# Kernel optimization log

Measured on AMD Instinct MI355X. Metric: run time of the kernel, lower is better.

The kernel has to match this reference:

```python
import jax, jax.numpy as jnp
import numpy as np

BETA = 0.25
EPS = 1e-10


def setup_inputs() -> dict:
    key = jax.random.key(0)
    k1, k2 = jax.random.split(key)
    B, D, K = 32768, 512, 8192
    a = jax.random.normal(k1, (B, D), dtype=jnp.float32)
    # torch init: uniform(-1/K, 1/K)
    codebook = jax.random.uniform(k2, (K, D), dtype=jnp.float32,
                                  minval=-1.0 / K, maxval=1.0 / K)
    return {"a": a, "codebook": codebook}


def reference(a, codebook):
    # a: [B, D], codebook: [K, D]
    B = a.shape[0]
    K = codebook.shape[0]
    # squared-distance via a2 + e2 - 2*a.E^T (no [B,K,D] intermediate)
    a2 = jnp.sum(a * a, axis=1, keepdims=True)            # [B, 1]
    e2 = jnp.sum(codebook * codebook, axis=1)[None, :]    # [1, K]
    dist = a2 + e2 - 2.0 * (a @ codebook.T)               # [B, K]
    idx = jnp.argmin(dist, axis=1)                        # [B] int
    z_q = codebook[idx]                                   # [B, D]
    # straight-through estimator
    z = a + jax.lax.stop_gradient(z_q - a)
    commit_loss = BETA * jnp.mean((a - jax.lax.stop_gradient(z_q)) ** 2)
    codebook_loss = jnp.mean((jax.lax.stop_gradient(a) - z_q) ** 2)
    # usage stats (no_grad in torch)
    usage = jnp.zeros((K,), a.dtype).at[idx].add(1.0) / B  # mean of one-hot
    perplexity = jnp.exp(-jnp.sum(usage * jnp.log(usage + EPS)))
    used_codes = jnp.sum(usage > 0).astype(a.dtype)
    usage_mean = jnp.mean(usage)
    return (idx, z, commit_loss, codebook_loss, perplexity, used_codes, usage_mean)
```

## Files before the change

kernel.cpp:

```cpp
#include <hip/hip_runtime.h>
#include <stdint.h>

#define D_DIM 512
#define ESTRIDE 528
#define SPLIT_K 384
#define DELTA 8.0e-4f
#define MAXC 48

typedef unsigned long long u64;
typedef float f32x4 __attribute__((ext_vector_type(4)));
typedef short s16x8 __attribute__((ext_vector_type(8)));

static __device__ inline unsigned short f2bf(float x) {
  unsigned u = __float_as_uint(x);
  u = (u + 0x7FFFu + ((u >> 16) & 1u)) >> 16;
  return (unsigned short)u;
}
static __device__ inline unsigned mono(float f) {
  unsigned u = __float_as_uint(f);
  return (u & 0x80000000u) ? ~u : (u | 0x80000000u);
}
static __device__ inline float unmono(unsigned m) {
  return __uint_as_float((m & 0x80000000u) ? (m & 0x7FFFFFFFu) : ~m);
}

__global__ void k_init(int* __restrict__ counts, int K) {
  int i = blockIdx.x * blockDim.x + threadIdx.x;
  if (i < K) counts[i] = 0;
}

__global__ void k_rowsq(const float* __restrict__ X, float* __restrict__ out, int nrows) {
  int t = threadIdx.x;
  int row = blockIdx.x * 4 + (t >> 6);
  int l = t & 63;
  if (row >= nrows) return;
  int b = l >> 4;
  int L = l & 15;
  const float* p = X + (size_t)row * D_DIM + b * 128 + L;
  float v[8];
#pragma unroll
  for (int j = 0; j < 8; ++j) {
    float x = p[16 * j];
    float sq = x * x;
    asm volatile("" : "+v"(sq));
    v[j] = sq;
  }
  float s = ((v[0] + v[1]) + (v[2] + v[3])) + ((v[4] + v[5]) + (v[6] + v[7]));
  s += __shfl_xor(s, 8, 64);
  s += __shfl_xor(s, 4, 64);
  s += __shfl_xor(s, 2, 64);
  s += __shfl_xor(s, 1, 64);
  s += __shfl_xor(s, 16, 64);
  s += __shfl_xor(s, 32, 64);
  if (l == 0) out[row] = s;
}

__global__ void k_ebf(const float* __restrict__ E, unsigned short* __restrict__ Ebf, int n8) {
  int i = blockIdx.x * blockDim.x + threadIdx.x;
  if (i >= n8) return;
  const float4 f0 = ((const float4*)E)[i * 2];
  const float4 f1 = ((const float4*)E)[i * 2 + 1];
  s16x8 o;
  o[0] = (short)f2bf(f0.x); o[1] = (short)f2bf(f0.y);
  o[2] = (short)f2bf(f0.z); o[3] = (short)f2bf(f0.w);
  o[4] = (short)f2bf(f1.x); o[5] = (short)f2bf(f1.y);
  o[6] = (short)f2bf(f1.z); o[7] = (short)f2bf(f1.w);
  ((s16x8*)Ebf)[i] = o;
}

__global__ void k_eskew(const float* __restrict__ E, float* __restrict__ Es, int n4) {
  int i = blockIdx.x * blockDim.x + threadIdx.x;
  if (i >= n4) return;
  int row = i >> 7;
  int c = i & 127;
  float4 v = ((const float4*)(E + (size_t)row * D_DIM))[c];
  ((float4*)(Es + (size_t)row * ESTRIDE))[c] = v;
}

__global__ __launch_bounds__(512) void k_screen(
    const float* __restrict__ A, const unsigned short* __restrict__ Ebf,
    const float* __restrict__ e2, int* __restrict__ cand_cnt,
    unsigned short* __restrict__ cand, int K) {
  __shared__ unsigned runmin[128];
  __shared__ unsigned cnt[128];
  __shared__ unsigned short list[128 * MAXC];
  __shared__ __align__(16) char Alds[128 * 1024];

  const int t = threadIdx.x;
  const int m0 = blockIdx.x * 128;

  if (t < 128) { runmin[t] = 0xFFFFFFFFu; cnt[t] = 0; }

  {
    int row = t >> 2;
    int s4 = t & 3;
    const float* ar = A + (size_t)(m0 + row) * D_DIM;
#pragma unroll
    for (int c = 0; c < 16; ++c) {
      int ch = s4 * 16 + c;
      float4 f0 = *(const float4*)(ar + ch * 8);
      float4 f1 = *(const float4*)(ar + ch * 8 + 4);
      s16x8 o;
      o[0] = (short)f2bf(f0.x); o[1] = (short)f2bf(f0.y);
      o[2] = (short)f2bf(f0.z); o[3] = (short)f2bf(f0.w);
      o[4] = (short)f2bf(f1.x); o[5] = (short)f2bf(f1.y);
      o[6] = (short)f2bf(f1.z); o[7] = (short)f2bf(f1.w);
      int off = ((row * 64 + ch) * 16) ^ ((row & 7) << 4);
      *(s16x8*)(Alds + off) = o;
    }
  }
  __syncthreads();

  const int lane = t & 63;
  const int wid = t >> 6;
  const int wm = wid >> 2;
  const int wn = wid & 3;
  const int l15 = lane & 15;
  const int lhi = lane >> 4;

  for (int n0 = 0; n0 < K; n0 += 128) {
    f32x4 acc[4][2];
#pragma unroll
    for (int r = 0; r < 4; ++r)
#pragma unroll
      for (int c = 0; c < 2; ++c) acc[r][c] = (f32x4){0.f, 0.f, 0.f, 0.f};
    const unsigned short* B0 = Ebf + (size_t)(n0 + wn * 32 + l15) * D_DIM + lhi * 8;
    const unsigned short* B1 = B0 + 16 * D_DIM;
#pragma unroll
    for (int dk = 0; dk < 16; ++dk) {
      s16x8 b0 = *(const s16x8*)(B0 + dk * 32);
      s16x8 b1 = *(const s16x8*)(B1 + dk * 32);
      s16x8 af[4];
#pragma unroll
      for (int r = 0; r < 4; ++r) {
        int row = wm * 64 + r * 16 + l15;
        int off = ((row * 64 + dk * 4 + lhi) * 16) ^ ((row & 7) << 4);
        af[r] = *(const s16x8*)(Alds + off);
      }
#pragma unroll
      for (int r = 0; r < 4; ++r) {
        acc[r][0] = __builtin_amdgcn_mfma_f32_16x16x32_bf16(af[r], b0, acc[r][0], 0, 0, 0);
        acc[r][1] = __builtin_amdgcn_mfma_f32_16x16x32_bf16(af[r], b1, acc[r][1], 0, 0, 0);
      }
    }
    float e2c0 = e2[n0 + wn * 32 + l15];
    float e2c1 = e2[n0 + wn * 32 + 16 + l15];
#pragma unroll
    for (int r = 0; r < 4; ++r)
#pragma unroll
      for (int g = 0; g < 4; ++g) {
        float s0 = fmaf(-2.f, acc[r][0][g], e2c0);
        float s1 = fmaf(-2.f, acc[r][1][g], e2c1);
        int row = wm * 64 + r * 16 + lhi * 4 + g;
        float mn = fminf(s0, s1);
        mn = fminf(mn, __shfl_xor(mn, 1, 64));
        mn = fminf(mn, __shfl_xor(mn, 2, 64));
        mn = fminf(mn, __shfl_xor(mn, 4, 64));
        mn = fminf(mn, __shfl_xor(mn, 8, 64));
        if (l15 == 0) atomicMin(&runmin[row], mono(mn));
        float thr = unmono(runmin[row]) + DELTA;
        if (s0 <= thr) {
          unsigned p = atomicAdd(&cnt[row], 1u);
          if (p < MAXC) list[row * MAXC + p] = (unsigned short)(n0 + wn * 32 + l15);
        }
        if (s1 <= thr) {
          unsigned p = atomicAdd(&cnt[row], 1u);
          if (p < MAXC) list[row * MAXC + p] = (unsigned short)(n0 + wn * 32 + 16 + l15);
        }
      }
  }
  __syncthreads();
  {
    int row = t >> 2;
    unsigned c = cnt[row];
    if ((t & 3) == 0) cand_cnt[m0 + row] = (int)c;
    unsigned cc = c < MAXC ? c : MAXC;
    for (unsigned p = t & 3; p < cc; p += 4)
      cand[(size_t)(m0 + row) * MAXC + p] = list[row * MAXC + p];
  }
}

static __device__ inline u64 exact_pack(const float* __restrict__ ar,
                                        const float* __restrict__ er,
                                        float a2r, float e2k, int k) {
  float acc1 = 0.f, acc2 = 0.f;
  for (int d = 0; d < SPLIT_K; d += 4) {
    float4 a = *(const float4*)(ar + d);
    float4 e = *(const float4*)(er + d);
    acc1 = fmaf(a.x, e.x, acc1); acc1 = fmaf(a.y, e.y, acc1);
    acc1 = fmaf(a.z, e.z, acc1); acc1 = fmaf(a.w, e.w, acc1);
  }
  for (int d = SPLIT_K; d < D_DIM; d += 4) {
    float4 a = *(const float4*)(ar + d);
    float4 e = *(const float4*)(er + d);
    acc2 = fmaf(a.x, e.x, acc2); acc2 = fmaf(a.y, e.y, acc2);
    acc2 = fmaf(a.z, e.z, acc2); acc2 = fmaf(a.w, e.w, acc2);
  }
  float M = acc1 + acc2;
  float S = a2r + e2k;
  float s = fmaf(-2.f, M, S);
  return ((u64)mono(s) << 32) | (unsigned)k;
}

__global__ __launch_bounds__(256) void k_rescore(
    const float* __restrict__ A, const float* __restrict__ Eskew,
    const float* __restrict__ a2, const float* __restrict__ e2,
    const int* __restrict__ cand_cnt, const unsigned short* __restrict__ cand,
    float* __restrict__ out_idx, float* __restrict__ out_z,
    float* __restrict__ rowsum, int* __restrict__ counts, int K) {
  int lane = threadIdx.x & 63;
  int r = blockIdx.x * 4 + (threadIdx.x >> 6);
  int c = cand_cnt[r];
  const float* ar = A + (size_t)r * D_DIM;
  float a2r = a2[r];
  u64 best = ~0ULL;
  if (c <= MAXC) {
    if (lane < c) {
      int k = cand[(size_t)r * MAXC + lane];
      best = exact_pack(ar, Eskew + (size_t)k * ESTRIDE, a2r, e2[k], k);
    }
  } else {
    for (int k = lane; k < K; k += 64) {
      u64 p = exact_pack(ar, Eskew + (size_t)k * ESTRIDE, a2r, e2[k], k);
      if (p < best) best = p;
    }
  }
#pragma unroll
  for (int m = 1; m < 64; m <<= 1) {
    u64 o = __shfl_xor(best, m, 64);
    if (o < best) best = o;
  }
  int idx = (int)(unsigned)(best & 0xFFFFFFFFULL);

  const float4* pa = (const float4*)(ar) + lane * 2;
  const float4* pe = (const float4*)(Eskew + (size_t)idx * ESTRIDE) + lane * 2;
  float4* pz = (float4*)(out_z + (size_t)r * D_DIM) + lane * 2;
  float ls = 0.f;
#pragma unroll
  for (int q = 0; q < 2; ++q) {
    float4 a = pa[q];
    float4 e = pe[q];
    float4 z;
    z.x = a.x + (e.x - a.x);
    z.y = a.y + (e.y - a.y);
    z.z = a.z + (e.z - a.z);
    z.w = a.w + (e.w - a.w);
    pz[q] = z;
    float dx = a.x - e.x, dy = a.y - e.y, dz = a.z - e.z, dw = a.w - e.w;
    ls += dx * dx + dy * dy + dz * dz + dw * dw;
  }
#pragma unroll
  for (int m = 1; m < 64; m <<= 1) ls += __shfl_xor(ls, m, 64);
  if (lane == 0) {
    out_idx[r] = (float)idx;
    rowsum[r] = ls;
    atomicAdd(&counts[idx], 1);
  }
}

#define KTILE(D0, ACC)                                                          \
  {                                                                             \
    int r = t >> 2;                                                             \
    int c4 = (t & 3) << 2;                                                      \
    float4 va = *(const float4*)(A + (size_t)(m0 + r) * D_DIM + (D0) + c4);     \
    As[c4 + 0][r] = va.x; As[c4 + 1][r] = va.y;                                 \
    As[c4 + 2][r] = va.z; As[c4 + 3][r] = va.w;                                 \
    float4 vb = *(const float4*)(E + (size_t)(n0 + r) * D_DIM + (D0) + c4);     \
    Es[c4 + 0][r] = vb.x; Es[c4 + 1][r] = vb.y;                                 \
    Es[c4 + 2][r] = vb.z; Es[c4 + 3][r] = vb.w;                                 \
    __syncthreads();                                                            \
    _Pragma("unroll")                                                           \
    for (int dd = 0; dd < 16; ++dd) {                                           \
      float af[4], bf[8];                                                       \
      *(float4*)af = *(const float4*)(&As[dd][ty * 4]);                         \
      *(float4*)bf = *(const float4*)(&Es[dd][tx * 4]);                         \
      *(float4*)(bf + 4) = *(const float4*)(&Es[dd][64 + tx * 4]);              \
      _Pragma("unroll")                                                         \
      for (int i = 0; i < 4; ++i)                                               \
        _Pragma("unroll")                                                       \
        for (int j = 0; j < 8; ++j)                                             \
          ACC[i][j] = fmaf(af[i], bf[j], ACC[i][j]);                            \
    }                                                                           \
    __syncthreads();                                                            \
  }

__global__ __launch_bounds__(512) void k_argmin_f32(
    const float* __restrict__ A, const float* __restrict__ E,
    const float* __restrict__ a2, const float* __restrict__ e2,
    float* __restrict__ out_idx, int* __restrict__ idx_ws, int K) {
  __shared__ float As[16][128];
  __shared__ float Es[16][128];
  const int m0 = blockIdx.x * 128;
  const int t = threadIdx.x;
  const int tx = t & 15;
  const int ty = t >> 4;
  float a2l[4];
#pragma unroll
  for (int i = 0; i < 4; ++i) a2l[i] = a2[m0 + ty * 4 + i];
  u64 best[4];
#pragma unroll
  for (int i = 0; i < 4; ++i) best[i] = ~0ULL;
  for (int n0 = 0; n0 < K; n0 += 128) {
    float acc1[4][8], acc2[4][8];
#pragma unroll
    for (int i = 0; i < 4; ++i)
#pragma unroll
      for (int j = 0; j < 8; ++j) { acc1[i][j] = 0.f; acc2[i][j] = 0.f; }
    for (int d0 = 0; d0 < SPLIT_K; d0 += 16) KTILE(d0, acc1)
    for (int d0 = SPLIT_K; d0 < D_DIM; d0 += 16) KTILE(d0, acc2)
    float e2l[8];
#pragma unroll
    for (int j = 0; j < 8; ++j) {
      int cl = (j < 4) ? (tx * 4 + j) : (64 + tx * 4 + (j - 4));
      e2l[j] = e2[n0 + cl];
    }
#pragma unroll
    for (int i = 0; i < 4; ++i) {
#pragma unroll
      for (int j = 0; j < 8; ++j) {
        int cl = (j < 4) ? (tx * 4 + j) : (64 + tx * 4 + (j - 4));
        float S = a2l[i] + e2l[j];
        float m = acc1[i][j] + acc2[i][j];
        float s = fmaf(-2.f, m, S);
        u64 p = ((u64)mono(s) << 32) | (unsigned)(n0 + cl);
        if (p < best[i]) best[i] = p;
      }
    }
  }
#pragma unroll
  for (int m = 1; m < 16; m <<= 1) {
#pragma unroll
    for (int i = 0; i < 4; ++i) {
      u64 o = __shfl_xor(best[i], m, 64);
      if (o < best[i]) best[i] = o;
    }
  }
  if (tx == 0) {
#pragma unroll
    for (int i = 0; i < 4; ++i) {
      int row = m0 + ty * 4 + i;
      int idx = (int)(unsigned)(best[i] & 0xFFFFFFFFULL);
      out_idx[row] = (float)idx;
      idx_ws[row] = idx;
    }
  }
}

__global__ void k_gather(const float* __restrict__ A, const float* __restrict__ E,
                         const int* __restrict__ idx_ws,
                         float* __restrict__ out_z, float* __restrict__ rowsum,
                         int* __restrict__ counts) {
  int b = blockIdx.x;
  int t = threadIdx.x;
  int idx = idx_ws[b];
  const float4* pa = (const float4*)(A + (size_t)b * D_DIM);
  const float4* pe = (const float4*)(E + (size_t)idx * D_DIM);
  float4 a = pa[t];
  float4 e = pe[t];
  float4 z;
  z.x = a.x + (e.x - a.x);
  z.y = a.y + (e.y - a.y);
  z.z = a.z + (e.z - a.z);
  z.w = a.w + (e.w - a.w);
  ((float4*)(out_z + (size_t)b * D_DIM))[t] = z;
  float dx = a.x - e.x, dy = a.y - e.y, dz = a.z - e.z, dw = a.w - e.w;
  float ls = dx * dx + dy * dy + dz * dz + dw * dw;
#pragma unroll
  for (int off = 32; off > 0; off >>= 1) ls += __shfl_down(ls, off, 64);
  __shared__ float wsum[2];
  if ((t & 63) == 0) wsum[t >> 6] = ls;
  __syncthreads();
  if (t == 0) {
    rowsum[b] = wsum[0] + wsum[1];
    atomicAdd(&counts[idx], 1);
  }
}

__global__ void k_stats(const int* __restrict__ counts, const float* __restrict__ rowsum,
                        float* __restrict__ out_sc, int B, int K) {
  int t = threadIdx.x;
  double ent = 0.0, tot = 0.0, S = 0.0;
  int used = 0;
  for (int k = t; k < K; k += 256) {
    int c = counts[k];
    double u = (double)c / (double)B;
    ent += u * log(u + 1e-10);
    tot += u;
    used += (c > 0) ? 1 : 0;
  }
  for (int b = t; b < B; b += 256) S += (double)rowsum[b];
  __shared__ double se[256];
  __shared__ double st[256];
  __shared__ double ss[256];
  __shared__ int su[256];
  se[t] = ent; st[t] = tot; ss[t] = S; su[t] = used;
  __syncthreads();
  for (int s = 128; s > 0; s >>= 1) {
    if (t < s) { se[t] += se[t + s]; st[t] += st[t + s]; ss[t] += ss[t + s]; su[t] += su[t + s]; }
    __syncthreads();
  }
  if (t == 0) {
    double Sm = ss[0];
    double N = (double)B * (double)D_DIM;
    out_sc[0] = (float)(0.25 * Sm / N);
    out_sc[1] = (float)(Sm / N);
    out_sc[2] = (float)exp(-se[0]);
    out_sc[3] = (float)su[0];
    out_sc[4] = (float)(st[0] / (double)K);
  }
}

extern "C" void kernel_launch(void* const* d_in, const int* in_sizes, int n_in,
                              void* d_out, int out_size, void* d_ws, size_t ws_size,
                              hipStream_t stream) {
  const float* A = (const float*)d_in[0];
  const float* E = (const float*)d_in[1];
  const int B = in_sizes[0] / D_DIM;
  const int K = in_sizes[1] / D_DIM;

  float* out = (float*)d_out;
  float* out_idx = out;
  float* out_z = out + B;
  float* out_sc = out + B + (size_t)B * D_DIM;

  char* ws = (char*)d_ws;
  size_t off = 0;
  float* a2 = (float*)(ws + off); off += (size_t)B * 4;
  float* e2 = (float*)(ws + off); off += (size_t)K * 4;
  int* counts = (int*)(ws + off); off += (size_t)K * 4;
  float* rowsum = (float*)(ws + off); off += (size_t)B * 4;
  int* idx_ws = (int*)(ws + off); off += (size_t)B * 4;
  int* cand_cnt = (int*)(ws + off); off += (size_t)B * 4;
  unsigned short* cand = (unsigned short*)(ws + off); off += (size_t)B * MAXC * 2;
  unsigned short* Ebf = (unsigned short*)(ws + off); off += (size_t)K * D_DIM * 2;
  float* Eskew = (float*)(ws + off); off += (size_t)K * ESTRIDE * 4;
  const size_t need = off;

  k_init<<<(K + 255) / 256, 256, 0, stream>>>(counts, K);
  k_rowsq<<<(B + 3) / 4, 256, 0, stream>>>(A, a2, B);
  k_rowsq<<<(K + 3) / 4, 256, 0, stream>>>(E, e2, K);

  if (ws_size >= need) {
    int n8 = K * D_DIM / 8;
    k_ebf<<<(n8 + 255) / 256, 256, 0, stream>>>(E, Ebf, n8);
    int n4 = K * D_DIM / 4;
    k_eskew<<<(n4 + 255) / 256, 256, 0, stream>>>(E, Eskew, n4);
    k_screen<<<B / 128, 512, 0, stream>>>(A, Ebf, e2, cand_cnt, cand, K);
    k_rescore<<<B / 4, 256, 0, stream>>>(A, Eskew, a2, e2, cand_cnt, cand,
                                         out_idx, out_z, rowsum, counts, K);
  } else {
    k_argmin_f32<<<B / 128, 512, 0, stream>>>(A, E, a2, e2, out_idx, idx_ws, K);
    k_gather<<<B, 128, 0, stream>>>(A, E, idx_ws, out_z, rowsum, counts);
  }
  k_stats<<<1, 256, 0, stream>>>(counts, rowsum, out_sc, B, K);
}
```

Before: 1.039 ms.

## Pad bf16 codebook rows, prefetch B fragments, widen LDS swizzle, cap occupancy

The bf16 codebook copy now uses a padded row stride of 544 elements, likely to avoid cache-channel or bank aliasing on strided row loads. In the screening kernel, all 16 k-steps of B fragments are loaded into registers before the MFMA loop, so global loads are issued together rather than interleaved with compute. The A tile LDS XOR swizzle is widened from 8 to 16 rows to cut bank conflicts. Launch bounds now request 2 blocks per CU, which raises register pressure alongside the 32 extra vector registers of prefetched fragments.

```diff
diff --git a/kernel.cpp b/kernel.cpp
--- a/kernel.cpp
+++ b/kernel.cpp
@@ -2,6 +2,7 @@
 #include <stdint.h>
 
 #define D_DIM 512
+#define EBFS 544
 #define ESTRIDE 528
 #define SPLIT_K 384
 #define DELTA 8.0e-4f
@@ -58,14 +59,16 @@
 __global__ void k_ebf(const float* __restrict__ E, unsigned short* __restrict__ Ebf, int n8) {
   int i = blockIdx.x * blockDim.x + threadIdx.x;
   if (i >= n8) return;
-  const float4 f0 = ((const float4*)E)[i * 2];
-  const float4 f1 = ((const float4*)E)[i * 2 + 1];
+  int row = i >> 6;
+  int ch = i & 63;
+  const float4 f0 = *(const float4*)(E + (size_t)row * D_DIM + ch * 8);
+  const float4 f1 = *(const float4*)(E + (size_t)row * D_DIM + ch * 8 + 4);
   s16x8 o;
   o[0] = (short)f2bf(f0.x); o[1] = (short)f2bf(f0.y);
   o[2] = (short)f2bf(f0.z); o[3] = (short)f2bf(f0.w);
   o[4] = (short)f2bf(f1.x); o[5] = (short)f2bf(f1.y);
   o[6] = (short)f2bf(f1.z); o[7] = (short)f2bf(f1.w);
-  ((s16x8*)Ebf)[i] = o;
+  *(s16x8*)(Ebf + (size_t)row * EBFS + ch * 8) = o;
 }
 
 __global__ void k_eskew(const float* __restrict__ E, float* __restrict__ Es, int n4) {
@@ -77,7 +80,7 @@
   ((float4*)(Es + (size_t)row * ESTRIDE))[c] = v;
 }
 
-__global__ __launch_bounds__(512) void k_screen(
+__global__ __launch_bounds__(512, 2) void k_screen(
     const float* __restrict__ A, const unsigned short* __restrict__ Ebf,
     const float* __restrict__ e2, int* __restrict__ cand_cnt,
     unsigned short* __restrict__ cand, int K) {
@@ -105,7 +108,7 @@
       o[2] = (short)f2bf(f0.z); o[3] = (short)f2bf(f0.w);
       o[4] = (short)f2bf(f1.x); o[5] = (short)f2bf(f1.y);
       o[6] = (short)f2bf(f1.z); o[7] = (short)f2bf(f1.w);
-      int off = ((row * 64 + ch) * 16) ^ ((row & 7) << 4);
+      int off = ((row * 64 + ch) * 16) ^ ((row & 15) << 4);
       *(s16x8*)(Alds + off) = o;
     }
   }
@@ -119,28 +122,34 @@
   const int lhi = lane >> 4;
 
   for (int n0 = 0; n0 < K; n0 += 128) {
+    s16x8 bb0[16], bb1[16];
+    {
+      const unsigned short* B0 = Ebf + (size_t)(n0 + wn * 32 + l15) * EBFS + lhi * 8;
+      const unsigned short* B1 = B0 + 16 * EBFS;
+#pragma unroll
+      for (int dk = 0; dk < 16; ++dk) {
+        bb0[dk] = *(const s16x8*)(B0 + dk * 32);
+        bb1[dk] = *(const s16x8*)(B1 + dk * 32);
+      }
+    }
     f32x4 acc[4][2];
 #pragma unroll
     for (int r = 0; r < 4; ++r)
 #pragma unroll
       for (int c = 0; c < 2; ++c) acc[r][c] = (f32x4){0.f, 0.f, 0.f, 0.f};
-    const unsigned short* B0 = Ebf + (size_t)(n0 + wn * 32 + l15) * D_DIM + lhi * 8;
-    const unsigned short* B1 = B0 + 16 * D_DIM;
 #pragma unroll
     for (int dk = 0; dk < 16; ++dk) {
-      s16x8 b0 = *(const s16x8*)(B0 + dk * 32);
-      s16x8 b1 = *(const s16x8*)(B1 + dk * 32);
       s16x8 af[4];
 #pragma unroll
       for (int r = 0; r < 4; ++r) {
         int row = wm * 64 + r * 16 + l15;
-        int off = ((row * 64 + dk * 4 + lhi) * 16) ^ ((row & 7) << 4);
+        int off = ((row * 64 + dk * 4 + lhi) * 16) ^ ((row & 15) << 4);
         af[r] = *(const s16x8*)(Alds + off);
       }
 #pragma unroll
       for (int r = 0; r < 4; ++r) {
-        acc[r][0] = __builtin_amdgcn_mfma_f32_16x16x32_bf16(af[r], b0, acc[r][0], 0, 0, 0);
-        acc[r][1] = __builtin_amdgcn_mfma_f32_16x16x32_bf16(af[r], b1, acc[r][1], 0, 0, 0);
+        acc[r][0] = __builtin_amdgcn_mfma_f32_16x16x32_bf16(af[r], bb0[dk], acc[r][0], 0, 0, 0);
+        acc[r][1] = __builtin_amdgcn_mfma_f32_16x16x32_bf16(af[r], bb1[dk], acc[r][1], 0, 0, 0);
       }
     }
     float e2c0 = e2[n0 + wn * 32 + l15];
@@ -432,7 +441,7 @@
   int* idx_ws = (int*)(ws + off); off += (size_t)B * 4;
   int* cand_cnt = (int*)(ws + off); off += (size_t)B * 4;
   unsigned short* cand = (unsigned short*)(ws + off); off += (size_t)B * MAXC * 2;
-  unsigned short* Ebf = (unsigned short*)(ws + off); off += (size_t)K * D_DIM * 2;
+  unsigned short* Ebf = (unsigned short*)(ws + off); off += (size_t)K * EBFS * 2;
   float* Eskew = (float*)(ws + off); off += (size_t)K * ESTRIDE * 4;
   const size_t need = off;
 
```

Result: faster. 910.2 us (-12.4%).

## Stage codebook tiles into LDS via async global_load_lds with double buffering

Applied to the files above, without the earlier changes.

The screening GEMM now streams pre-tiled bf16 codebook chunks into a double-buffered LDS region using global_load_lds, instead of each wave reading B fragments straight from global memory. A new prep kernel writes the codebook in a chunk-major tiled layout and, in the same pass, produces the fp32 skewed copy and zeroes the counts, replacing three small launches. The A swizzle is widened to reduce LDS bank conflicts. The tile loop is hardcoded to K=8192, and a block-wide barrier now runs every k-step, which adds sync overhead.

```diff
diff --git a/kernel.cpp b/kernel.cpp
--- a/kernel.cpp
+++ b/kernel.cpp
@@ -27,6 +27,29 @@
 __global__ void k_init(int* __restrict__ counts, int K) {
   int i = blockIdx.x * blockDim.x + threadIdx.x;
   if (i < K) counts[i] = 0;
+}
+
+__global__ void k_prep(const float* __restrict__ E, unsigned short* __restrict__ Ebf2,
+                       float* __restrict__ Eskew, int* __restrict__ counts, int K) {
+  int i = blockIdx.x * blockDim.x + threadIdx.x;
+  if (i < K) counts[i] = 0;
+  if (i >= K * 64) return;
+  int row = i >> 6;
+  int ch = i & 63;
+  const float* src = E + (size_t)row * D_DIM + ch * 8;
+  float4 f0 = *(const float4*)(src);
+  float4 f1 = *(const float4*)(src + 4);
+  s16x8 o;
+  o[0] = (short)f2bf(f0.x); o[1] = (short)f2bf(f0.y);
+  o[2] = (short)f2bf(f0.z); o[3] = (short)f2bf(f0.w);
+  o[4] = (short)f2bf(f1.x); o[5] = (short)f2bf(f1.y);
+  o[6] = (short)f2bf(f1.z); o[7] = (short)f2bf(f1.w);
+  size_t slot = ((size_t)(row >> 7) * 16 + (size_t)(ch >> 2)) * 512 +
+                (size_t)(row & 127) * 4 + (size_t)(ch & 3);
+  *(s16x8*)(Ebf2 + slot * 8) = o;
+  float* dst = Eskew + (size_t)row * ESTRIDE + ch * 8;
+  *(float4*)(dst) = f0;
+  *(float4*)(dst + 4) = f1;
 }
 
 __global__ void k_rowsq(const float* __restrict__ X, float* __restrict__ out, int nrows) {
@@ -55,36 +78,15 @@
   if (l == 0) out[row] = s;
 }
 
-__global__ void k_ebf(const float* __restrict__ E, unsigned short* __restrict__ Ebf, int n8) {
-  int i = blockIdx.x * blockDim.x + threadIdx.x;
-  if (i >= n8) return;
-  const float4 f0 = ((const float4*)E)[i * 2];
-  const float4 f1 = ((const float4*)E)[i * 2 + 1];
-  s16x8 o;
-  o[0] = (short)f2bf(f0.x); o[1] = (short)f2bf(f0.y);
-  o[2] = (short)f2bf(f0.z); o[3] = (short)f2bf(f0.w);
-  o[4] = (short)f2bf(f1.x); o[5] = (short)f2bf(f1.y);
-  o[6] = (short)f2bf(f1.z); o[7] = (short)f2bf(f1.w);
-  ((s16x8*)Ebf)[i] = o;
-}
-
-__global__ void k_eskew(const float* __restrict__ E, float* __restrict__ Es, int n4) {
-  int i = blockIdx.x * blockDim.x + threadIdx.x;
-  if (i >= n4) return;
-  int row = i >> 7;
-  int c = i & 127;
-  float4 v = ((const float4*)(E + (size_t)row * D_DIM))[c];
-  ((float4*)(Es + (size_t)row * ESTRIDE))[c] = v;
-}
-
 __global__ __launch_bounds__(512) void k_screen(
-    const float* __restrict__ A, const unsigned short* __restrict__ Ebf,
+    const float* __restrict__ A, const unsigned short* __restrict__ Ebf2,
     const float* __restrict__ e2, int* __restrict__ cand_cnt,
     unsigned short* __restrict__ cand, int K) {
   __shared__ unsigned runmin[128];
   __shared__ unsigned cnt[128];
   __shared__ unsigned short list[128 * MAXC];
   __shared__ __align__(16) char Alds[128 * 1024];
+  __shared__ __align__(16) char Blds[2 * 8192];
 
   const int t = threadIdx.x;
   const int m0 = blockIdx.x * 128;
@@ -105,11 +107,10 @@
       o[2] = (short)f2bf(f0.z); o[3] = (short)f2bf(f0.w);
       o[4] = (short)f2bf(f1.x); o[5] = (short)f2bf(f1.y);
       o[6] = (short)f2bf(f1.z); o[7] = (short)f2bf(f1.w);
-      int off = ((row * 64 + ch) * 16) ^ ((row & 7) << 4);
+      int off = ((row * 64 + ch) * 16) ^ ((row & 15) << 4);
       *(s16x8*)(Alds + off) = o;
     }
   }
-  __syncthreads();
 
   const int lane = t & 63;
   const int wid = t >> 6;
@@ -118,23 +119,40 @@
   const int l15 = lane & 15;
   const int lhi = lane >> 4;
 
-  for (int n0 = 0; n0 < K; n0 += 128) {
+#define ISSUE_CHUNK(C)                                                          \
+  {                                                                             \
+    const unsigned short* _src = Ebf2 + ((size_t)(C) * 512 + t) * 8;            \
+    __builtin_amdgcn_global_load_lds(                                           \
+        (const __attribute__((address_space(1))) unsigned int*)_src,            \
+        (__attribute__((address_space(3))) unsigned int*)(Blds + ((C) & 1) * 8192 + wid * 1024), \
+        16, 0, 0);                                                              \
+  }
+
+  ISSUE_CHUNK(0)
+  __syncthreads();
+
+  for (int tile = 0; tile < 64; ++tile) {
+    const int n0 = tile * 128;
+
     f32x4 acc[4][2];
 #pragma unroll
     for (int r = 0; r < 4; ++r)
 #pragma unroll
       for (int c = 0; c < 2; ++c) acc[r][c] = (f32x4){0.f, 0.f, 0.f, 0.f};
-    const unsigned short* B0 = Ebf + (size_t)(n0 + wn * 32 + l15) * D_DIM + lhi * 8;
-    const unsigned short* B1 = B0 + 16 * D_DIM;
-#pragma unroll
-    for (int dk = 0; dk < 16; ++dk) {
-      s16x8 b0 = *(const s16x8*)(B0 + dk * 32);
-      s16x8 b1 = *(const s16x8*)(B1 + dk * 32);
+
+#pragma unroll
+    for (int kk = 0; kk < 16; ++kk) {
+      const int c = tile * 16 + kk;
+      if (c + 1 < 1024) ISSUE_CHUNK(c + 1)
+
+      const char* Bc = Blds + (c & 1) * 8192;
+      s16x8 b0 = *(const s16x8*)(Bc + ((wn * 32 + l15) * 4 + lhi) * 16);
+      s16x8 b1 = *(const s16x8*)(Bc + ((wn * 32 + 16 + l15) * 4 + lhi) * 16);
       s16x8 af[4];
 #pragma unroll
       for (int r = 0; r < 4; ++r) {
         int row = wm * 64 + r * 16 + l15;
-        int off = ((row * 64 + dk * 4 + lhi) * 16) ^ ((row & 7) << 4);
+        int off = ((row * 64 + kk * 4 + lhi) * 16) ^ ((row & 15) << 4);
         af[r] = *(const s16x8*)(Alds + off);
       }
 #pragma unroll
@@ -142,7 +160,9 @@
         acc[r][0] = __builtin_amdgcn_mfma_f32_16x16x32_bf16(af[r], b0, acc[r][0], 0, 0, 0);
         acc[r][1] = __builtin_amdgcn_mfma_f32_16x16x32_bf16(af[r], b1, acc[r][1], 0, 0, 0);
       }
-    }
+      __syncthreads();
+    }
+
     float e2c0 = e2[n0 + wn * 32 + l15];
     float e2c1 = e2[n0 + wn * 32 + 16 + l15];
 #pragma unroll
@@ -432,23 +452,21 @@
   int* idx_ws = (int*)(ws + off); off += (size_t)B * 4;
   int* cand_cnt = (int*)(ws + off); off += (size_t)B * 4;
   unsigned short* cand = (unsigned short*)(ws + off); off += (size_t)B * MAXC * 2;
-  unsigned short* Ebf = (unsigned short*)(ws + off); off += (size_t)K * D_DIM * 2;
+  unsigned short* Ebf2 = (unsigned short*)(ws + off); off += (size_t)K * 512 * 2;
   float* Eskew = (float*)(ws + off); off += (size_t)K * ESTRIDE * 4;
   const size_t need = off;
 
-  k_init<<<(K + 255) / 256, 256, 0, stream>>>(counts, K);
   k_rowsq<<<(B + 3) / 4, 256, 0, stream>>>(A, a2, B);
   k_rowsq<<<(K + 3) / 4, 256, 0, stream>>>(E, e2, K);
 
   if (ws_size >= need) {
-    int n8 = K * D_DIM / 8;
-    k_ebf<<<(n8 + 255) / 256, 256, 0, stream>>>(E, Ebf, n8);
-    int n4 = K * D_DIM / 4;
-    k_eskew<<<(n4 + 255) / 256, 256, 0, stream>>>(E, Eskew, n4);
-    k_screen<<<B / 128, 512, 0, stream>>>(A, Ebf, e2, cand_cnt, cand, K);
+    int np = K * 64;
+    k_prep<<<(np + 255) / 256, 256, 0, stream>>>(E, Ebf2, Eskew, counts, K);
+    k_screen<<<B / 128, 512, 0, stream>>>(A, Ebf2, e2, cand_cnt, cand, K);
     k_rescore<<<B / 4, 256, 0, stream>>>(A, Eskew, a2, e2, cand_cnt, cand,
                                          out_idx, out_z, rowsum, counts, K);
   } else {
+    k_init<<<(K + 255) / 256, 256, 0, stream>>>(counts, K);
     k_argmin_f32<<<B / 128, 512, 0, stream>>>(A, E, a2, e2, out_idx, idx_ws, K);
     k_gather<<<B, 128, 0, stream>>>(A, E, idx_ws, out_z, rowsum, counts);
   }
```

Result: slower. 1.078 ms (+3.7%).
